# Optimization experiments

Hardware: AMD Instinct MI355X
Metric: run time of the kernel (lower is better)

## Reference

```python
import jax, jax.numpy as jnp
import numpy as np

IMAGE_TOKEN = 32000
PAD_TOKEN = 0
IGNORE_INDEX = -100
PATCH = 14
B, S = 8, 1024
IMG = 336
VOCAB = 32064
D = 4096          # text embed_dim
DV = 1024         # vision hidden
N_LAYERS, N_EXPERTS, N_SHARED = 32, 8, 2
NP = (IMG // PATCH) ** 2          # 576 patches after dropping CLS
MAXE = (NP - 1) + S               # one <image> token per row -> 1599


def setup_inputs() -> dict:
    key = jax.random.key(0)
    ks = jax.random.split(key, 12)
    input_ids = jax.random.randint(ks[0], (B, S), 1, IMAGE_TOKEN)  # avoid pad(0) and image token
    input_ids = input_ids.at[:, 5].set(IMAGE_TOKEN)                # exactly one image token per row
    pixel_values = jax.random.normal(ks[1], (B, 3, IMG, IMG), jnp.float32)
    attention_mask = jnp.ones((B, S), jnp.int32)
    labels = jax.random.randint(ks[2], (B, S), 0, IMAGE_TOKEN)
    embed_table = jax.random.normal(ks[3], (VOCAB, D), jnp.float32) * 0.02
    cls_emb = jax.random.normal(ks[4], (DV,), jnp.float32) * 0.02
    patch_w = jax.random.normal(ks[5], (3 * PATCH * PATCH, DV), jnp.float32) * 0.02
    patch_b = jax.random.normal(ks[6], (DV,), jnp.float32) * 0.02
    proj_w1 = jax.random.normal(ks[7], (DV, D), jnp.float32) * 0.02
    proj_b1 = jax.random.normal(ks[8], (D,), jnp.float32) * 0.02
    proj_w2 = jax.random.normal(ks[9], (D, D), jnp.float32) * 0.02
    proj_b2 = jax.random.normal(ks[10], (D,), jnp.float32) * 0.02
    return dict(input_ids=input_ids, pixel_values=pixel_values, attention_mask=attention_mask,
                labels=labels, embed_table=embed_table, cls_emb=cls_emb, patch_w=patch_w,
                patch_b=patch_b, proj_w1=proj_w1, proj_b1=proj_b1, proj_w2=proj_w2, proj_b2=proj_b2)


def _vision_project(pixel_values, cls_emb, patch_w, patch_b, w1, b1, w2, b2):
    # Vision tower stub: patchify + linear patch embedding, CLS prepended,
    # then 'default' select strategy drops CLS, then 2-layer GELU projector.
    n = pixel_values.shape[0]
    g = IMG // PATCH
    x = pixel_values.reshape(n, 3, g, PATCH, g, PATCH)
    x = x.transpose(0, 2, 4, 1, 3, 5).reshape(n, g * g, 3 * PATCH * PATCH)
    h = x @ patch_w + patch_b                                   # [n, 576, DV]
    hidden = jnp.concatenate([jnp.broadcast_to(cls_emb, (n, 1, DV)), h], axis=1)  # [n, 577, DV]
    sel = hidden[:, 1:]                                          # drop CLS ('default')
    return jax.nn.gelu(sel @ w1 + b1) @ w2 + b2                  # [n, 576, D]


def _merge(image_features, inputs_embeds, input_ids, attention_mask, labels):
    b, s = input_ids.shape
    n, p, d = image_features.shape
    special = input_ids == IMAGE_TOKEN                           # [B,S]
    left_padding = jnp.sum(input_ids[:, -1] == PAD_TOKEN) == 0
    new_pos = jnp.cumsum(special.astype(jnp.int32) * (p - 1) + 1, axis=-1) - 1
    nb_pad = MAXE - 1 - new_pos[:, -1]
    new_pos = new_pos + jnp.where(left_padding, nb_pad[:, None], 0)
    pos_safe = jnp.where(special, MAXE, new_pos)                 # OOB index for image tokens -> dropped
    bi = jnp.arange(b)[:, None]
    final_emb = jnp.zeros((b, MAXE, d), inputs_embeds.dtype).at[bi, pos_safe].set(inputs_embeds, mode='drop')
    final_attn = jnp.zeros((b, MAXE), attention_mask.dtype).at[bi, pos_safe].set(attention_mask, mode='drop')
    final_labels = jnp.full((b, MAXE), IGNORE_INDEX, labels.dtype).at[bi, pos_safe].set(labels, mode='drop')
    img_ow = jnp.all(final_emb == 0, axis=-1)                    # slots never written by text
    img_ow = img_ow & (jnp.cumsum(img_ow.astype(jnp.int32), axis=-1) - 1 >= nb_pad[:, None])
    flat_mask = img_ow.reshape(-1)                               # [B*MAXE]
    rank = jnp.cumsum(flat_mask.astype(jnp.int32)) - 1           # row-major rank of each True slot
    img_flat = image_features.reshape(-1, d)                     # [n*p, D]
    gathered = img_flat[jnp.clip(rank, 0, img_flat.shape[0] - 1)]
    final_emb = jnp.where(flat_mask[:, None], gathered, final_emb.reshape(-1, d)).reshape(b, MAXE, d)
    final_attn = jnp.where(img_ow, jnp.ones_like(final_attn), final_attn)
    return final_emb, final_attn, final_labels


def reference(input_ids, pixel_values, attention_mask, labels, embed_table, cls_emb,
              patch_w, patch_b, proj_w1, proj_b1, proj_w2, proj_b2):
    inputs_embeds = embed_table[input_ids]                       # [B,S,D]
    image_features = _vision_project(pixel_values, cls_emb, patch_w, patch_b,
                                     proj_w1, proj_b1, proj_w2, proj_b2)
    final_emb, final_attn, final_labels = _merge(image_features, inputs_embeds,
                                                 input_ids, attention_mask, labels)
    # torch.empty buffers (uninitialized scratch) -> zeros for determinism
    router_logits = jnp.zeros((N_LAYERS, MAXE, N_EXPERTS), jnp.float32)
    shared_router_logits = jnp.zeros((N_LAYERS, MAXE, N_SHARED), jnp.float32)
    current_layer = jnp.int32(0)
    return (current_layer, final_emb, final_attn, final_labels, router_logits, shared_router_logits)
```

## Files before the change

kernel.cpp:

```cpp
#include <hip/hip_runtime.h>
#include <math.h>

#define B_ 8
#define S_ 1024
#define D_ 4096
#define DV_ 1024
#define NP_ 576
#define MAXE_ 1599
#define PK_ 588
#define KP_ 608
#define IMG_ 336
#define GRID_ 24
#define PATCH_ 14
#define IMAGE_TOKEN_ 32000
#define PAD_TOKEN_ 0
#define NLAYERS_ 32
#define NEXP_ 8
#define NSH_ 2

#define EMB_ELEMS ((size_t)B_ * MAXE_ * D_)
#define OFF_EMB   ((size_t)1)
#define OFF_ATTN  (OFF_EMB + EMB_ELEMS)
#define OFF_LAB   (OFF_ATTN + (size_t)B_ * MAXE_)
#define OFF_ROUTER (OFF_LAB + (size_t)B_ * MAXE_)
#define ROUTER_ELEMS ((size_t)NLAYERS_ * MAXE_ * (NEXP_ + NSH_))

typedef __bf16 bf16x8 __attribute__((ext_vector_type(8)));
typedef float  f32x4  __attribute__((ext_vector_type(4)));
typedef unsigned short ushort_t;

__device__ __forceinline__ unsigned short f2bf(float f) {
    unsigned u = __float_as_uint(f);
    u += 0x7fffu + ((u >> 16) & 1u);
    return (unsigned short)(u >> 16);
}

__device__ __forceinline__ float bf2f(unsigned short u) {
    return __uint_as_float((unsigned)u << 16);
}

__device__ __forceinline__ void async_copy16(const void* g, void* l) {
    __builtin_amdgcn_global_load_lds(
        (const __attribute__((address_space(1))) void*)g,
        (__attribute__((address_space(3))) void*)l, 16, 0, 0);
}

__global__ void fill_tail_kernel(float* __restrict__ out) {
    size_t i = (size_t)blockIdx.x * blockDim.x + threadIdx.x;
    if (i == 0) out[0] = 0.0f;
    for (size_t j = i; j < ROUTER_ELEMS; j += (size_t)gridDim.x * blockDim.x)
        out[OFF_ROUTER + j] = 0.0f;
}

__global__ __launch_bounds__(512) void merge_kernel(
    const int* __restrict__ input_ids, const int* __restrict__ attn_mask,
    const int* __restrict__ labels, float* __restrict__ out,
    int* __restrict__ src_index, int* __restrict__ img_pos)
{
    __shared__ int sh_nbpad[B_];
    __shared__ int sh_shift[B_];
    __shared__ int sh_nqual[B_];
    __shared__ int sh_leftpad;
    float* out_attn = out + OFF_ATTN;
    float* out_lab  = out + OFF_LAB;
    const int tid = threadIdx.x;

    for (int i = tid; i < B_ * MAXE_; i += blockDim.x) {
        src_index[i] = -1;
        out_attn[i] = 0.0f;
        out_lab[i] = -100.0f;
    }
    for (int i = tid; i < B_ * NP_; i += blockDim.x) img_pos[i] = -1;
    if (tid == 0) {
        int anypad = 0;
        for (int b = 0; b < B_; b++)
            if (input_ids[b * S_ + S_ - 1] == PAD_TOKEN_) anypad = 1;
        sh_leftpad = !anypad;
    }
    __syncthreads();

    const int wave = tid >> 6;
    const int lane = tid & 63;
    const unsigned long long below = (1ull << lane) - 1ull;

    if (wave < B_) {
        const int b = wave;
        int nspec = 0;
        for (int c = 0; c < S_; c += 64) {
            int id = input_ids[b * S_ + c + lane];
            nspec += __popcll(__ballot(id == IMAGE_TOKEN_));
        }
        int nb_pad = MAXE_ - S_ - (NP_ - 1) * nspec;
        int shift = sh_leftpad ? nb_pad : 0;
        int nholes = MAXE_ - (S_ - nspec);
        int nq = nholes - nb_pad; if (nq < 0) nq = 0;
        if (lane == 0) { sh_nbpad[b] = nb_pad; sh_shift[b] = shift; sh_nqual[b] = nq; }
        int carry = 0;
        for (int c = 0; c < S_; c += 64) {
            int t = c + lane;
            int id = input_ids[b * S_ + t];
            int spec = (id == IMAGE_TOKEN_);
            unsigned long long m = __ballot(spec);
            int nbefore = carry + __popcll(m & below);
            if (!spec) {
                int pos = t + (NP_ - 1) * nbefore + shift;
                if (pos >= 0 && pos < MAXE_) {
                    src_index[b * MAXE_ + pos] = t;
                    out_attn[b * MAXE_ + pos] = (float)attn_mask[b * S_ + t];
                    out_lab[b * MAXE_ + pos]  = (float)labels[b * S_ + t];
                }
            }
            carry += __popcll(m);
        }
    }
    __syncthreads();

    if (wave < B_) {
        const int b = wave;
        int offs = 0;
        for (int r = 0; r < b; r++) offs += sh_nqual[r];
        const int nb_pad = sh_nbpad[b];
        int hcarry = 0;
        for (int c = 0; c < MAXE_; c += 64) {
            int p = c + lane;
            int flag = 0;
            if (p < MAXE_) flag = (src_index[b * MAXE_ + p] == -1);
            unsigned long long m = __ballot(flag);
            int h = hcarry + __popcll(m & below);
            if (flag && h >= nb_pad) {
                int g = offs + (h - nb_pad);
                if (g > B_ * NP_ - 1) g = B_ * NP_ - 1;
                if (g < 0) g = 0;
                img_pos[g] = b * MAXE_ + p;
                src_index[b * MAXE_ + p] = -2;
                out_attn[b * MAXE_ + p] = 1.0f;
            }
            hcarry += __popcll(m);
        }
    }
}

__global__ void patchify_split_kernel(const float* __restrict__ pix,
                                      ushort_t* __restrict__ xh,
                                      ushort_t* __restrict__ xl)
{
    int i = blockIdx.x * blockDim.x + threadIdx.x;
    const int total = B_ * NP_ * KP_;
    if (i >= total) return;
    int q = i % KP_;
    int t = (i / KP_) % NP_;
    int n = i / (KP_ * NP_);
    float v = 0.0f;
    if (q < PK_) {
        int c = q / (PATCH_ * PATCH_);
        int r = q % (PATCH_ * PATCH_);
        int py = r / PATCH_, px = r % PATCH_;
        int gy = t / GRID_, gx = t % GRID_;
        v = pix[(((size_t)n * 3 + c) * IMG_ + gy * PATCH_ + py) * IMG_ + gx * PATCH_ + px];
    }
    ushort_t h = f2bf(v);
    xh[i] = h;
    xl[i] = f2bf(v - bf2f(h));
}

__global__ __launch_bounds__(256) void transpose_bf16_kernel(
    const float* __restrict__ src, ushort_t* __restrict__ dst, int R, int C)
{
    __shared__ float tile[32][33];
    int c0 = blockIdx.x * 32, r0 = blockIdx.y * 32;
    int tx = threadIdx.x & 31, ty = threadIdx.x >> 5;
    for (int i = ty; i < 32; i += 8)
        tile[i][tx] = src[(size_t)(r0 + i) * C + c0 + tx];
    __syncthreads();
    for (int i = ty; i < 32; i += 8)
        dst[(size_t)(c0 + i) * R + r0 + tx] = f2bf(tile[tx][i]);
}

__global__ __launch_bounds__(256) void transpose_split_kernel(
    const float* __restrict__ src, ushort_t* __restrict__ dh,
    ushort_t* __restrict__ dl, int R, int C, int RP)
{
    __shared__ float tile[32][33];
    int c0 = blockIdx.x * 32, r0 = blockIdx.y * 32;
    int tx = threadIdx.x & 31, ty = threadIdx.x >> 5;
    for (int i = ty; i < 32; i += 8) {
        float v = 0.0f;
        if (r0 + i < R && c0 + tx < C) v = src[(size_t)(r0 + i) * C + c0 + tx];
        tile[i][tx] = v;
    }
    __syncthreads();
    for (int i = ty; i < 32; i += 8) {
        if (c0 + i < C && r0 + tx < RP) {
            float v = tile[tx][i];
            ushort_t h = f2bf(v);
            dh[(size_t)(c0 + i) * RP + r0 + tx] = h;
            dl[(size_t)(c0 + i) * RP + r0 + tx] = f2bf(v - bf2f(h));
        }
    }
}

__global__ __launch_bounds__(256) void mfma_gemm_split(
    const ushort_t* __restrict__ Ah, const ushort_t* __restrict__ Al,
    const ushort_t* __restrict__ Bth, const ushort_t* __restrict__ Btl,
    const float* __restrict__ bias, ushort_t* __restrict__ outb,
    int M, int N, int K)
{
    __shared__ ushort_t Ash[128 * 32];
    __shared__ ushort_t Asl[128 * 32];
    __shared__ ushort_t Bsh[128 * 32];
    __shared__ ushort_t Bsl[128 * 32];
    const int tid  = threadIdx.x;
    const int wave = tid >> 6;
    const int lane = tid & 63;
    const int l16  = lane & 15;
    const int quad = lane >> 4;
    const int wrow = (wave >> 1) * 64;
    const int wcol = (wave & 1) * 64;
    const int row0 = blockIdx.y * 128;
    const int col0 = blockIdx.x * 128;

    f32x4 acc[4][4];
#pragma unroll
    for (int i = 0; i < 4; i++)
#pragma unroll
        for (int j = 0; j < 4; j++) acc[i][j] = (f32x4)(0.0f);

    const int R0a = wave * 32;
    const int lr  = lane >> 2;
    const int lc  = (lane & 3) * 8;

    for (int k0 = 0; k0 < K; k0 += 32) {
#pragma unroll
        for (int i = 0; i < 2; i++) {
            int R0 = R0a + i * 16;
            size_t aoff = (size_t)(row0 + R0 + lr) * K + k0 + lc;
            size_t boff = (size_t)(col0 + R0 + lr) * K + k0 + lc;
            async_copy16(Ah  + aoff, &Ash[R0 * 32]);
            async_copy16(Al  + aoff, &Asl[R0 * 32]);
            async_copy16(Bth + boff, &Bsh[R0 * 32]);
            async_copy16(Btl + boff, &Bsl[R0 * 32]);
        }
        __syncthreads();

        bf16x8 ah[4], al[4], bh[4], bl[4];
#pragma unroll
        for (int mt = 0; mt < 4; mt++) {
            ah[mt] = *(const bf16x8*)&Ash[(wrow + mt * 16 + l16) * 32 + quad * 8];
            al[mt] = *(const bf16x8*)&Asl[(wrow + mt * 16 + l16) * 32 + quad * 8];
        }
#pragma unroll
        for (int nt = 0; nt < 4; nt++) {
            bh[nt] = *(const bf16x8*)&Bsh[(wcol + nt * 16 + l16) * 32 + quad * 8];
            bl[nt] = *(const bf16x8*)&Bsl[(wcol + nt * 16 + l16) * 32 + quad * 8];
        }
#pragma unroll
        for (int mt = 0; mt < 4; mt++)
#pragma unroll
            for (int nt = 0; nt < 4; nt++) {
                acc[mt][nt] = __builtin_amdgcn_mfma_f32_16x16x32_bf16(
                    ah[mt], bh[nt], acc[mt][nt], 0, 0, 0);
                acc[mt][nt] = __builtin_amdgcn_mfma_f32_16x16x32_bf16(
                    ah[mt], bl[nt], acc[mt][nt], 0, 0, 0);
                acc[mt][nt] = __builtin_amdgcn_mfma_f32_16x16x32_bf16(
                    al[mt], bh[nt], acc[mt][nt], 0, 0, 0);
            }
        __syncthreads();
    }

    float bv[4];
#pragma unroll
    for (int nt = 0; nt < 4; nt++) bv[nt] = bias[col0 + wcol + nt * 16 + l16];

#pragma unroll
    for (int mt = 0; mt < 4; mt++) {
#pragma unroll
        for (int r = 0; r < 4; r++) {
            int row = row0 + wrow + mt * 16 + quad * 4 + r;
            ushort_t* dst = outb + (size_t)row * N;
#pragma unroll
            for (int nt = 0; nt < 4; nt++) {
                int col = col0 + wcol + nt * 16 + l16;
                dst[col] = f2bf(acc[mt][nt][r] + bv[nt]);
            }
        }
    }
}

__global__ __launch_bounds__(256) void mfma_gemm_bt(
    const ushort_t* __restrict__ A, const ushort_t* __restrict__ Bt,
    const float* __restrict__ bias, ushort_t* __restrict__ outb,
    float* __restrict__ outf, const int* __restrict__ pos_map,
    int M, int N, int K, int mode)
{
    __shared__ ushort_t As[128 * 32];
    __shared__ ushort_t Bs[128 * 32];
    const int tid  = threadIdx.x;
    const int wave = tid >> 6;
    const int lane = tid & 63;
    const int l16  = lane & 15;
    const int quad = lane >> 4;
    const int wrow = (wave >> 1) * 64;
    const int wcol = (wave & 1) * 64;
    const int row0 = blockIdx.y * 128;
    const int col0 = blockIdx.x * 128;

    f32x4 acc[4][4];
#pragma unroll
    for (int i = 0; i < 4; i++)
#pragma unroll
        for (int j = 0; j < 4; j++) acc[i][j] = (f32x4)(0.0f);

    const int R0a = wave * 32;
    const int lr  = lane >> 2;
    const int lc  = (lane & 3) * 8;

    for (int k0 = 0; k0 < K; k0 += 32) {
#pragma unroll
        for (int i = 0; i < 2; i++) {
            int R0 = R0a + i * 16;
            const ushort_t* ga = A  + (size_t)(row0 + R0 + lr) * K + k0 + lc;
            const ushort_t* gb = Bt + (size_t)(col0 + R0 + lr) * K + k0 + lc;
            async_copy16(ga, &As[R0 * 32]);
            async_copy16(gb, &Bs[R0 * 32]);
        }
        __syncthreads();

        bf16x8 af[4], bf[4];
#pragma unroll
        for (int mt = 0; mt < 4; mt++)
            af[mt] = *(const bf16x8*)&As[(wrow + mt * 16 + l16) * 32 + quad * 8];
#pragma unroll
        for (int nt = 0; nt < 4; nt++)
            bf[nt] = *(const bf16x8*)&Bs[(wcol + nt * 16 + l16) * 32 + quad * 8];
#pragma unroll
        for (int mt = 0; mt < 4; mt++)
#pragma unroll
            for (int nt = 0; nt < 4; nt++)
                acc[mt][nt] = __builtin_amdgcn_mfma_f32_16x16x32_bf16(
                    af[mt], bf[nt], acc[mt][nt], 0, 0, 0);
        __syncthreads();
    }

    float bv[4];
#pragma unroll
    for (int nt = 0; nt < 4; nt++) bv[nt] = bias[col0 + wcol + nt * 16 + l16];

#pragma unroll
    for (int mt = 0; mt < 4; mt++) {
#pragma unroll
        for (int r = 0; r < 4; r++) {
            int row = row0 + wrow + mt * 16 + quad * 4 + r;
            if (mode == 2) {
                int orow = pos_map[row];
                if (orow < 0) continue;
#pragma unroll
                for (int nt = 0; nt < 4; nt++) {
                    int col = col0 + wcol + nt * 16 + l16;
                    outf[(size_t)orow * N + col] = acc[mt][nt][r] + bv[nt];
                }
            } else {
#pragma unroll
                for (int nt = 0; nt < 4; nt++) {
                    int col = col0 + wcol + nt * 16 + l16;
                    float x = acc[mt][nt][r] + bv[nt];
                    float u = 0.7978845608028654f * (x + 0.044715f * x * x * x);
                    x = x / (1.0f + __expf(-2.0f * u));
                    outb[(size_t)row * N + col] = f2bf(x);
                }
            }
        }
    }
}

__global__ __launch_bounds__(256) void scatter_text_kernel(
    const int* __restrict__ src_index, const int* __restrict__ input_ids,
    const float* __restrict__ embed, float* __restrict__ final_emb)
{
    int row = blockIdx.x;
    int src = src_index[row];
    if (src == -2) return;
    float4* dst = (float4*)(final_emb + (size_t)row * D_);
    if (src >= 0) {
        int b = row / MAXE_;
        int tok = input_ids[b * S_ + src];
        const float4* s = (const float4*)(embed + (size_t)tok * D_);
#pragma unroll
        for (int i = threadIdx.x; i < D_ / 4; i += 256) dst[i] = s[i];
    } else {
#pragma unroll
        for (int i = threadIdx.x; i < D_ / 4; i += 256)
            dst[i] = make_float4(0.f, 0.f, 0.f, 0.f);
    }
}

extern "C" void kernel_launch(void* const* d_in, const int* in_sizes, int n_in,
                              void* d_out, int out_size, void* d_ws, size_t ws_size,
                              hipStream_t stream)
{
    const int*   input_ids = (const int*)d_in[0];
    const float* pixel     = (const float*)d_in[1];
    const int*   attn      = (const int*)d_in[2];
    const int*   labels    = (const int*)d_in[3];
    const float* embed     = (const float*)d_in[4];
    const float* patch_w   = (const float*)d_in[6];
    const float* patch_b   = (const float*)d_in[7];
    const float* w1        = (const float*)d_in[8];
    const float* b1        = (const float*)d_in[9];
    const float* w2        = (const float*)d_in[10];
    const float* b2        = (const float*)d_in[11];
    float* out = (float*)d_out;

    char* w = (char*)d_ws;
    int* src_index = (int*)w;
    int* img_pos   = (int*)(w + 51200);
    ushort_t* xh   = (ushort_t*)(w + 51200 + 18432);
    ushort_t* xl   = xh  + (size_t)B_ * NP_ * KP_;
    ushort_t* pwh  = xl  + (size_t)B_ * NP_ * KP_;
    ushort_t* pwl  = pwh + (size_t)DV_ * KP_;
    ushort_t* hbuf = pwl + (size_t)DV_ * KP_;
    ushort_t* g1   = hbuf + (size_t)B_ * NP_ * DV_;
    ushort_t* w1t  = g1 + (size_t)B_ * NP_ * D_;
    ushort_t* w2t  = w1t + (size_t)D_ * DV_;

    fill_tail_kernel<<<2048, 256, 0, stream>>>(out);
    merge_kernel<<<1, 512, 0, stream>>>(input_ids, attn, labels, out, src_index, img_pos);

    {
        int total = B_ * NP_ * KP_;
        patchify_split_kernel<<<(total + 255) / 256, 256, 0, stream>>>(pixel, xh, xl);
    }
    transpose_split_kernel<<<dim3(DV_ / 32, KP_ / 32), 256, 0, stream>>>(
        patch_w, pwh, pwl, PK_, DV_, KP_);
    transpose_bf16_kernel<<<dim3(D_ / 32, DV_ / 32), 256, 0, stream>>>(w1, w1t, DV_, D_);
    transpose_bf16_kernel<<<dim3(D_ / 32, D_ / 32), 256, 0, stream>>>(w2, w2t, D_, D_);

    const int M = B_ * NP_;
    mfma_gemm_split<<<dim3(DV_ / 128, M / 128), 256, 0, stream>>>(
        xh, xl, pwh, pwl, patch_b, hbuf, M, DV_, KP_);
    mfma_gemm_bt<<<dim3(D_ / 128, M / 128), 256, 0, stream>>>(
        hbuf, w1t, b1, g1, nullptr, nullptr, M, D_, DV_, 1);
    mfma_gemm_bt<<<dim3(D_ / 128, M / 128), 256, 0, stream>>>(
        g1, w2t, b2, nullptr, out + OFF_EMB, img_pos, M, D_, D_, 2);

    scatter_text_kernel<<<B_ * MAXE_, 256, 0, stream>>>(src_index, input_ids, embed, out + OFF_EMB);
}
```

Baseline: 1.087 ms.

## Double K-tile depth, swizzle LDS layout, and remap blocks across XCDs in bf16 GEMM

```diff
diff --git a/kernel.cpp b/kernel.cpp
--- a/kernel.cpp
+++ b/kernel.cpp
@@ -292,8 +292,8 @@
     float* __restrict__ outf, const int* __restrict__ pos_map,
     int M, int N, int K, int mode)
 {
-    __shared__ ushort_t As[128 * 32];
-    __shared__ ushort_t Bs[128 * 32];
+    __shared__ ushort_t As[128 * 64];
+    __shared__ ushort_t Bs[128 * 64];
     const int tid  = threadIdx.x;
     const int wave = tid >> 6;
     const int lane = tid & 63;
@@ -301,8 +301,16 @@
     const int quad = lane >> 4;
     const int wrow = (wave >> 1) * 64;
     const int wcol = (wave & 1) * 64;
-    const int row0 = blockIdx.y * 128;
-    const int col0 = blockIdx.x * 128;
+
+    int nwg = gridDim.x;
+    int bid = blockIdx.x;
+    if ((nwg & 7) == 0) {
+        int cpx = nwg >> 3;
+        bid = (bid & 7) * cpx + (bid >> 3);
+    }
+    const int nbx = N >> 7;
+    const int row0 = (bid / nbx) * 128;
+    const int col0 = (bid % nbx) * 128;
 
     f32x4 acc[4][4];
 #pragma unroll
@@ -310,34 +318,44 @@
 #pragma unroll
         for (int j = 0; j < 4; j++) acc[i][j] = (f32x4)(0.0f);
 
-    const int R0a = wave * 32;
-    const int lr  = lane >> 2;
-    const int lc  = (lane & 3) * 8;
-
-    for (int k0 = 0; k0 < K; k0 += 32) {
-#pragma unroll
-        for (int i = 0; i < 2; i++) {
-            int R0 = R0a + i * 16;
-            const ushort_t* ga = A  + (size_t)(row0 + R0 + lr) * K + k0 + lc;
-            const ushort_t* gb = Bt + (size_t)(col0 + R0 + lr) * K + k0 + lc;
-            async_copy16(ga, &As[R0 * 32]);
-            async_copy16(gb, &Bs[R0 * 32]);
+    const int srow = lane >> 3;
+    const int scol = 8 * ((lane & 7) ^ srow);
+
+    for (int k0 = 0; k0 < K; k0 += 64) {
+#pragma unroll
+        for (int i = 0; i < 4; i++) {
+            int R0 = wave * 32 + i * 8;
+            const ushort_t* ga = A  + (size_t)(row0 + R0 + srow) * K + k0 + scol;
+            const ushort_t* gb = Bt + (size_t)(col0 + R0 + srow) * K + k0 + scol;
+            async_copy16(ga, &As[R0 * 64]);
+            async_copy16(gb, &Bs[R0 * 64]);
         }
         __syncthreads();
 
-        bf16x8 af[4], bf[4];
-#pragma unroll
-        for (int mt = 0; mt < 4; mt++)
-            af[mt] = *(const bf16x8*)&As[(wrow + mt * 16 + l16) * 32 + quad * 8];
-#pragma unroll
-        for (int nt = 0; nt < 4; nt++)
-            bf[nt] = *(const bf16x8*)&Bs[(wcol + nt * 16 + l16) * 32 + quad * 8];
-#pragma unroll
-        for (int mt = 0; mt < 4; mt++)
-#pragma unroll
-            for (int nt = 0; nt < 4; nt++)
-                acc[mt][nt] = __builtin_amdgcn_mfma_f32_16x16x32_bf16(
-                    af[mt], bf[nt], acc[mt][nt], 0, 0, 0);
+        bf16x8 af[4][2], bf[4][2];
+#pragma unroll
+        for (int s = 0; s < 2; s++) {
+#pragma unroll
+            for (int mt = 0; mt < 4; mt++) {
+                int r = wrow + mt * 16 + l16;
+                int pc = ((s << 2) + quad) ^ (l16 & 7);
+                af[mt][s] = *(const bf16x8*)&As[r * 64 + pc * 8];
+            }
+#pragma unroll
+            for (int nt = 0; nt < 4; nt++) {
+                int r = wcol + nt * 16 + l16;
+                int pc = ((s << 2) + quad) ^ (l16 & 7);
+                bf[nt][s] = *(const bf16x8*)&Bs[r * 64 + pc * 8];
+            }
+        }
+#pragma unroll
+        for (int s = 0; s < 2; s++)
+#pragma unroll
+            for (int mt = 0; mt < 4; mt++)
+#pragma unroll
+                for (int nt = 0; nt < 4; nt++)
+                    acc[mt][nt] = __builtin_amdgcn_mfma_f32_16x16x32_bf16(
+                        af[mt][s], bf[nt][s], acc[mt][nt], 0, 0, 0);
         __syncthreads();
     }
 
@@ -437,9 +455,9 @@
     const int M = B_ * NP_;
     mfma_gemm_split<<<dim3(DV_ / 128, M / 128), 256, 0, stream>>>(
         xh, xl, pwh, pwl, patch_b, hbuf, M, DV_, KP_);
-    mfma_gemm_bt<<<dim3(D_ / 128, M / 128), 256, 0, stream>>>(
+    mfma_gemm_bt<<<(D_ / 128) * (M / 128), 256, 0, stream>>>(
         hbuf, w1t, b1, g1, nullptr, nullptr, M, D_, DV_, 1);
-    mfma_gemm_bt<<<dim3(D_ / 128, M / 128), 256, 0, stream>>>(
+    mfma_gemm_bt<<<(D_ / 128) * (M / 128), 256, 0, stream>>>(
         g1, w2t, b2, nullptr, out + OFF_EMB, img_pos, M, D_, D_, 2);
 
     scatter_text_kernel<<<B_ * MAXE_, 256, 0, stream>>>(src_index, input_ids, embed, out + OFF_EMB);
```

New measurement: 1.111 ms. 2.1% more time.
